# Performance work log

Measured on AMD Instinct MI355X. Metric: run time of the kernel, lower is better.

Reference implementation:

```python
import jax, jax.numpy as jnp
import numpy as np

N = 100000   # nodes
E = 1600000  # edges
F_IN = 128
HID = 128
C = 40
EPS = 1e-5


def setup_inputs() -> dict:
    key = jax.random.key(0)
    ks = jax.random.split(key, 8)
    x = jax.random.normal(ks[0], (N, F_IN), dtype=jnp.float32)
    edge_index = jax.random.randint(ks[1], (2, E), 0, N, dtype=jnp.int32)
    s = 0.05
    return {
        "x": x,
        "edge_index": edge_index,
        "W1": jax.random.normal(ks[2], (F_IN, HID), dtype=jnp.float32) * s,
        "b1": jnp.zeros((HID,), jnp.float32),
        "g1": jnp.ones((HID,), jnp.float32),
        "be1": jnp.zeros((HID,), jnp.float32),
        "W2": jax.random.normal(ks[3], (HID, HID), dtype=jnp.float32) * s,
        "b2": jnp.zeros((HID,), jnp.float32),
        "g2": jnp.ones((HID,), jnp.float32),
        "be2": jnp.zeros((HID,), jnp.float32),
        "W3": jax.random.normal(ks[4], (HID, C), dtype=jnp.float32) * s,
        "b3": jnp.zeros((C,), jnp.float32),
    }


def _gcn_conv(x, W, b, src, dst, deg_inv_sqrt):
    # h = X W; then symmetric-normalized aggregation over edges (incl. self loops)
    h = x @ W                                  # [N, out]
    coef = deg_inv_sqrt[src] * deg_inv_sqrt[dst]  # [E+N]
    msg = h[src] * coef[:, None]               # gather + scale
    out = jax.ops.segment_sum(msg, dst, num_segments=N)
    return out + b


def _batchnorm(x, g, be):
    mean = jnp.mean(x, axis=0)
    var = jnp.mean(jnp.square(x - mean), axis=0)  # biased var (torch BN train)
    return (x - mean) * jax.lax.rsqrt(var + EPS) * g + be


def reference(x, edge_index, W1, b1, g1, be1, W2, b2, g2, be2, W3, b3):
    # add self loops once
    loop = jnp.arange(N, dtype=edge_index.dtype)
    src = jnp.concatenate([edge_index[0], loop])
    dst = jnp.concatenate([edge_index[1], loop])
    deg = jax.ops.segment_sum(jnp.ones_like(dst, dtype=x.dtype), dst, num_segments=N)
    dinv = jax.lax.rsqrt(deg)  # deg >= 1 due to self loops

    h = _gcn_conv(x, W1, b1, src, dst, dinv)
    h = _batchnorm(h, g1, be1)
    h = h + x                      # residual: hidden_dim == num_features
    h = jax.nn.relu(h)             # dropout: eval-mode identity

    h = _gcn_conv(h, W2, b2, src, dst, dinv)
    h = _batchnorm(h, g2, be2)
    h = jax.nn.relu(h)

    h = _gcn_conv(h, W3, b3, src, dst, dinv)
    return jax.nn.log_softmax(h, axis=1)
```

## Files before the change

### kernel.cpp

```cpp
#include <hip/hip_runtime.h>
#include <hip/hip_bf16.h>

#define NN 100000
#define EE 1600000
#define HID 128
#define CLS 40
#define EPSBN 1e-5f
#define NBUK ((NN + 255) >> 8)
#define CAP 6144
#define EPB 4096
#define NPB 512

typedef float f32x4 __attribute__((ext_vector_type(4)));
typedef float f32x2 __attribute__((ext_vector_type(2)));
typedef short s16x8 __attribute__((ext_vector_type(8)));
union U48 { uint4 u; s16x8 s; };

static __device__ __forceinline__ unsigned short f2bf(float f) {
    unsigned u = __float_as_uint(f);
    unsigned r = (u + 0x7fff + ((u >> 16) & 1)) >> 16;
    return (unsigned short)r;
}
static __device__ __forceinline__ unsigned pack2(float a, float b) {
    return (unsigned)f2bf(a) | ((unsigned)f2bf(b) << 16);
}
static __device__ __forceinline__ float bflo(unsigned v) { return __uint_as_float(v << 16); }
static __device__ __forceinline__ float bfhi(unsigned v) { return __uint_as_float(v & 0xffff0000u); }


__global__ void prep_all(const float* __restrict__ W1, const float* __restrict__ W2,
                         const float* __restrict__ W3,
                         unsigned* __restrict__ Wf1, unsigned* __restrict__ Wf2,
                         unsigned* __restrict__ Wf3,
                         int* gcur, float* stats1, float* stats2) {
    int blk = blockIdx.x;
    int tid = threadIdx.x;
    if (blk < 64) {
        const float* W = (blk < 32) ? W1 : W2;
        unsigned* Wf = (blk < 32) ? Wf1 : Wf2;
        int t = ((blk & 31) << 8) + tid;
        int q = t & 3, lane = (t >> 2) & 63, f = t >> 8;
        int ks = f >> 3, ct = f & 7;
        int k = ks * 32 + ((lane >> 4) << 3) + q * 2;
        int col = ct * 16 + (lane & 15);
        Wf[t] = pack2(W[k * 128 + col], W[(k + 1) * 128 + col]);
    } else if (blk < 76) {
        int t = ((blk - 64) << 8) + tid;
        int q = t & 3, lane = (t >> 2) & 63, f = t >> 8;
        int ks = f / 3, ct = f - ks * 3;
        int k = ks * 32 + ((lane >> 4) << 3) + q * 2;
        int col = ct * 16 + (lane & 15);
        float v0 = (col < CLS) ? W3[k * CLS + col] : 0.0f;
        float v1 = (col < CLS) ? W3[(k + 1) * CLS + col] : 0.0f;
        Wf3[t] = pack2(v0, v1);
    } else {
        int j = ((blk - 76) << 8) + tid;
        if (j < NBUK) gcur[j] = j * CAP;
        if (blk == 76) {
            stats1[tid] = 0.0f;
            stats2[tid] = 0.0f;
        }
    }
}


__global__ __launch_bounds__(256) void fill_p1_binned(const int* __restrict__ src,
                                                      const int* __restrict__ dst,
                                                      int* gcur, int* __restrict__ tmp) {
    __shared__ int cnt[NBUK];
    __shared__ int base[NBUK];
    int tid = threadIdx.x;
    for (int j = tid; j < NBUK; j += 256) cnt[j] = 0;
    __syncthreads();

    int es[16], ed[16];
    int i0 = blockIdx.x * EPB;
#pragma unroll
    for (int k = 0; k < 16; k++) {
        int i = i0 + k * 256 + tid;
        bool ok = i < EE;
        es[k] = ok ? src[i] : -1;
        ed[k] = ok ? dst[i] : 0;
        if (ok) atomicAdd(&cnt[ed[k] >> 8], 1);
    }
    __syncthreads();
    for (int j = tid; j < NBUK; j += 256) {
        int c = cnt[j];
        base[j] = c ? atomicAdd(&gcur[j], c) : 0;
        cnt[j] = 0;
    }
    __syncthreads();
#pragma unroll
    for (int k = 0; k < 16; k++) {
        if (es[k] >= 0) {
            int b = ed[k] >> 8;
            int r = atomicAdd(&cnt[b], 1);
            tmp[base[b] + r] = (es[k] << 8) | (ed[k] & 255);
        }
    }
}

__global__ __launch_bounds__(512) void bucket_scan(const int* __restrict__ gcur,
                                                   int* __restrict__ gbase,
                                                   int* __restrict__ row_ptr) {
    __shared__ int sc[512];
    int tid = threadIdx.x;
    int v = (tid < NBUK) ? gcur[tid] - tid * CAP : 0;
    sc[tid] = v;
    __syncthreads();
    for (int off = 1; off < 512; off <<= 1) {
        int t = (tid >= off) ? sc[tid - off] : 0;
        __syncthreads();
        sc[tid] += t;
        __syncthreads();
    }
    if (tid < NBUK) gbase[tid] = sc[tid] - v;
    if (tid == NBUK - 1) {
        gbase[NBUK] = sc[tid];
        row_ptr[NN] = sc[tid];
    }
}

__global__ __launch_bounds__(256) void fill_p2(const int* __restrict__ tmp,
                                               const int* __restrict__ gcur,
                                               const int* __restrict__ gbase,
                                               float* __restrict__ dinv,
                                               int* __restrict__ row_ptr,
                                               int* __restrict__ csr) {
    __shared__ int cnt[256];
    __shared__ int sc[256];
    __shared__ int cur[256];
    int b = blockIdx.x;
    int tid = threadIdx.x;
    int total = gcur[b] - b * CAP;
    cnt[tid] = 0;
    __syncthreads();
    int lo = b * CAP;
    for (int k = tid; k < total; k += 256) atomicAdd(&cnt[tmp[lo + k] & 255], 1);
    __syncthreads();
    int c = cnt[tid];
    sc[tid] = c;
    __syncthreads();
    for (int off = 1; off < 256; off <<= 1) {
        int t = (tid >= off) ? sc[tid - off] : 0;
        __syncthreads();
        sc[tid] += t;
        __syncthreads();
    }
    int node = (b << 8) + tid;
    int rp = gbase[b] + sc[tid] - c;
    if (node < NN) {
        dinv[node] = rsqrtf((float)(c + 1));
        row_ptr[node] = rp;
    }
    cur[tid] = rp;
    __syncthreads();
    for (int k = tid; k < total; k += 256) {
        int v = tmp[lo + k];
        int p = atomicAdd(&cur[v & 255], 1);
        csr[p] = ((unsigned)v) >> 8;
    }
}


template <int MODE>
__global__ __launch_bounds__(256) void gemm128_mfma(const float* __restrict__ Xf,
                                                    const unsigned* __restrict__ Xb,
                                                    const unsigned* __restrict__ Wf,
                                                    const float* __restrict__ stats,
                                                    const float* __restrict__ gam,
                                                    const float* __restrict__ bet,
                                                    const float* __restrict__ xres,
                                                    const float* __restrict__ dinv,
                                                    unsigned char* __restrict__ Hb) {
    int t = threadIdx.x;
    int lane = t & 63, w = t >> 6;
    int wr = w >> 1, wc = w & 1;
    int row_base = blockIdx.x * 64 + wr * 32;

    s16x8 b[4][4];
    const uint4* Wv = (const uint4*)Wf;
#pragma unroll
    for (int ks = 0; ks < 4; ks++)
#pragma unroll
        for (int ct = 0; ct < 4; ct++) {
            int f = ks * 8 + wc * 4 + ct;
            U48 u; u.u = Wv[f * 64 + lane];
            b[ks][ct] = u.s;
        }

    f32x4 acc[2][4] = {};
    int lrow = lane & 15;
    int koff = (lane >> 4) << 3;
    const float invN = 1.0f / (float)NN;

#pragma unroll
    for (int ks = 0; ks < 4; ks++) {
        int k0 = ks * 32 + koff;
        float sc[8], sh[8];
        if (MODE == 1) {
            float4 s0 = *(const float4*)&stats[k0];
            float4 s1 = *(const float4*)&stats[k0 + 4];
            float4 q0 = *(const float4*)&stats[128 + k0];
            float4 q1 = *(const float4*)&stats[128 + k0 + 4];
            float4 g0 = *(const float4*)&gam[k0];
            float4 g1 = *(const float4*)&gam[k0 + 4];
            float4 e0 = *(const float4*)&bet[k0];
            float4 e1 = *(const float4*)&bet[k0 + 4];
            float sv[8] = {s0.x,s0.y,s0.z,s0.w,s1.x,s1.y,s1.z,s1.w};
            float qv[8] = {q0.x,q0.y,q0.z,q0.w,q1.x,q1.y,q1.z,q1.w};
            float gv[8] = {g0.x,g0.y,g0.z,g0.w,g1.x,g1.y,g1.z,g1.w};
            float ev[8] = {e0.x,e0.y,e0.z,e0.w,e1.x,e1.y,e1.z,e1.w};
#pragma unroll
            for (int j = 0; j < 8; j++) {
                float mean = sv[j] * invN;
                float var = qv[j] * invN - mean * mean;
                sc[j] = gv[j] * rsqrtf(var + EPSBN);
                sh[j] = ev[j] - mean * sc[j];
            }
        }
#pragma unroll
        for (int rf = 0; rf < 2; rf++) {
            int row = row_base + rf * 16 + lrow;
            float v[8];
            if (row < NN) {
                if (MODE == 0) {
                    float4 a0 = *(const float4*)&Xf[(size_t)row * 128 + k0];
                    float4 a1 = *(const float4*)&Xf[(size_t)row * 128 + k0 + 4];
                    v[0]=a0.x; v[1]=a0.y; v[2]=a0.z; v[3]=a0.w;
                    v[4]=a1.x; v[5]=a1.y; v[6]=a1.z; v[7]=a1.w;
                } else {
                    uint4 u = *(const uint4*)&Xb[(size_t)row * 64 + k0 / 2];
                    v[0]=bflo(u.x); v[1]=bfhi(u.x); v[2]=bflo(u.y); v[3]=bfhi(u.y);
                    v[4]=bflo(u.z); v[5]=bfhi(u.z); v[6]=bflo(u.w); v[7]=bfhi(u.w);
                    float4 r0 = *(const float4*)&xres[(size_t)row * 128 + k0];
                    float4 r1 = *(const float4*)&xres[(size_t)row * 128 + k0 + 4];
                    float rr[8] = {r0.x,r0.y,r0.z,r0.w,r1.x,r1.y,r1.z,r1.w};
#pragma unroll
                    for (int j = 0; j < 8; j++)
                        v[j] = fmaxf(fmaf(v[j], sc[j], sh[j]) + rr[j], 0.0f);
                }
            } else {
#pragma unroll
                for (int j = 0; j < 8; j++) v[j] = 0.0f;
            }
            U48 a;
            a.u = make_uint4(pack2(v[0], v[1]), pack2(v[2], v[3]),
                             pack2(v[4], v[5]), pack2(v[6], v[7]));
#pragma unroll
            for (int ct = 0; ct < 4; ct++)
                acc[rf][ct] = __builtin_amdgcn_mfma_f32_16x16x32_bf16(a.s, b[ks][ct], acc[rf][ct], 0, 0, 0);
        }
    }

#pragma unroll
    for (int rf = 0; rf < 2; rf++) {
        int rbase = row_base + rf * 16 + ((lane >> 4) << 2);
        float dv[4];
#pragma unroll
        for (int r = 0; r < 4; r++) dv[r] = (rbase + r < NN) ? dinv[rbase + r] : 0.0f;
#pragma unroll
        for (int ct = 0; ct < 4; ct++) {
            int col = wc * 64 + ct * 16 + lrow;
#pragma unroll
            for (int r = 0; r < 4; r++) {
                int row = rbase + r;
                if (row < NN) {
                    int pv = __builtin_amdgcn_cvt_pk_fp8_f32(acc[rf][ct][r] * dv[r], 0.0f, 0, false);
                    Hb[(size_t)row * 128 + col] = (unsigned char)pv;
                }
            }
        }
    }
}

__global__ __launch_bounds__(256) void gemm40_mfma(const unsigned* __restrict__ Xb,
                                                   const unsigned* __restrict__ Wf,
                                                   const float* __restrict__ stats,
                                                   const float* __restrict__ gam,
                                                   const float* __restrict__ bet,
                                                   const float* __restrict__ dinv,
                                                   unsigned char* __restrict__ H3) {
    int t = threadIdx.x;
    int lane = t & 63, w = t >> 6;
    int row_base = blockIdx.x * 64 + w * 16;

    s16x8 b[4][3];
    const uint4* Wv = (const uint4*)Wf;
#pragma unroll
    for (int ks = 0; ks < 4; ks++)
#pragma unroll
        for (int ct = 0; ct < 3; ct++) {
            U48 u; u.u = Wv[(ks * 3 + ct) * 64 + lane];
            b[ks][ct] = u.s;
        }

    f32x4 acc[3] = {};
    int lrow = lane & 15;
    int koff = (lane >> 4) << 3;
    const float invN = 1.0f / (float)NN;

#pragma unroll
    for (int ks = 0; ks < 4; ks++) {
        int k0 = ks * 32 + koff;
        float4 s0 = *(const float4*)&stats[k0];
        float4 s1 = *(const float4*)&stats[k0 + 4];
        float4 q0 = *(const float4*)&stats[128 + k0];
        float4 q1 = *(const float4*)&stats[128 + k0 + 4];
        float4 g0 = *(const float4*)&gam[k0];
        float4 g1 = *(const float4*)&gam[k0 + 4];
        float4 e0 = *(const float4*)&bet[k0];
        float4 e1 = *(const float4*)&bet[k0 + 4];
        float sv[8] = {s0.x,s0.y,s0.z,s0.w,s1.x,s1.y,s1.z,s1.w};
        float qv[8] = {q0.x,q0.y,q0.z,q0.w,q1.x,q1.y,q1.z,q1.w};
        float gv[8] = {g0.x,g0.y,g0.z,g0.w,g1.x,g1.y,g1.z,g1.w};
        float ev[8] = {e0.x,e0.y,e0.z,e0.w,e1.x,e1.y,e1.z,e1.w};
        float sc[8], sh[8];
#pragma unroll
        for (int j = 0; j < 8; j++) {
            float mean = sv[j] * invN;
            float var = qv[j] * invN - mean * mean;
            sc[j] = gv[j] * rsqrtf(var + EPSBN);
            sh[j] = ev[j] - mean * sc[j];
        }
        int row = row_base + lrow;
        float v[8];
        if (row < NN) {
            uint4 u = *(const uint4*)&Xb[(size_t)row * 64 + k0 / 2];
            float av[8] = {bflo(u.x), bfhi(u.x), bflo(u.y), bfhi(u.y),
                           bflo(u.z), bfhi(u.z), bflo(u.w), bfhi(u.w)};
#pragma unroll
            for (int j = 0; j < 8; j++)
                v[j] = fmaxf(fmaf(av[j], sc[j], sh[j]), 0.0f);
        } else {
#pragma unroll
            for (int j = 0; j < 8; j++) v[j] = 0.0f;
        }
        U48 a;
        a.u = make_uint4(pack2(v[0], v[1]), pack2(v[2], v[3]),
                         pack2(v[4], v[5]), pack2(v[6], v[7]));
#pragma unroll
        for (int ct = 0; ct < 3; ct++)
            acc[ct] = __builtin_amdgcn_mfma_f32_16x16x32_bf16(a.s, b[ks][ct], acc[ct], 0, 0, 0);
    }

    int rbase = row_base + ((lane >> 4) << 2);
    float dv[4];
#pragma unroll
    for (int r = 0; r < 4; r++) dv[r] = (rbase + r < NN) ? dinv[rbase + r] : 0.0f;
#pragma unroll
    for (int ct = 0; ct < 3; ct++) {
        int col = ct * 16 + lrow;
        if (col >= CLS) continue;
#pragma unroll
        for (int r = 0; r < 4; r++) {
            int row = rbase + r;
            if (row < NN) {
                int pv = __builtin_amdgcn_cvt_pk_fp8_f32(acc[ct][r] * dv[r], 0.0f, 0, false);
                H3[(size_t)row * CLS + col] = (unsigned char)pv;
            }
        }
    }
}


__global__ __launch_bounds__(256) void agg128_half(const unsigned* __restrict__ h8,
                                                   const int* __restrict__ row_ptr,
                                                   const int* __restrict__ csr,
                                                   const float* __restrict__ dinv,
                                                   const float* __restrict__ bias,
                                                   uint2* __restrict__ outb) {
    int wid = threadIdx.x >> 6;
    int lane = threadIdx.x & 63;
    int half = lane >> 5, l = lane & 31;
    int node = blockIdx.x * 8 + wid * 2 + half;

    unsigned sv = h8[(size_t)node * 32 + l];
    f32x2 alo = __builtin_amdgcn_cvt_pk_f32_fp8(sv, false);
    f32x2 ahi = __builtin_amdgcn_cvt_pk_f32_fp8(sv, true);

    int beg = row_ptr[node], end = row_ptr[node + 1];
    int cnt = end - beg;
    int cmax = max(cnt, __shfl_xor(cnt, 32));

    for (int k = 0; k < cmax; k += 12) {
        int si[12];
        unsigned g[12];
#pragma unroll
        for (int j = 0; j < 12; j++) {
            int idx = beg + k + j;
            si[j] = csr[(idx < end) ? idx : beg];
        }
#pragma unroll
        for (int j = 0; j < 12; j++) {
            int idx = beg + k + j;
            g[j] = (idx < end) ? h8[(size_t)si[j] * 32 + l] : 0u;
        }
#pragma unroll
        for (int j = 0; j < 12; j++) {
            alo += __builtin_amdgcn_cvt_pk_f32_fp8(g[j], false);
            ahi += __builtin_amdgcn_cvt_pk_f32_fp8(g[j], true);
        }
    }

    float di = dinv[node];
    float4 b = *(const float4*)&bias[l * 4];
    outb[(size_t)node * 32 + l] =
        make_uint2(pack2(fmaf(alo.x, di, b.x), fmaf(alo.y, di, b.y)),
                   pack2(fmaf(ahi.x, di, b.z), fmaf(ahi.y, di, b.w)));
}

__global__ __launch_bounds__(256) void agg40_lsm(const unsigned* __restrict__ h3,
                                                 const int* __restrict__ row_ptr,
                                                 const int* __restrict__ csr,
                                                 const float* __restrict__ dinv,
                                                 const float* __restrict__ b3,
                                                 float* __restrict__ out) {
    int wid = threadIdx.x >> 6;
    int lane = threadIdx.x & 63;
    int half = lane >> 5, l30 = lane & 31;
    int slot = l30 / 10;
    int fp = l30 - slot * 10;
    bool sok = slot < 3;
    int node = blockIdx.x * 8 + wid * 2 + half;

    f32x2 alo = {0.0f, 0.0f}, ahi = {0.0f, 0.0f};
    if (slot == 0) {
        unsigned v = h3[(size_t)node * 10 + fp];
        alo = __builtin_amdgcn_cvt_pk_f32_fp8(v, false);
        ahi = __builtin_amdgcn_cvt_pk_f32_fp8(v, true);
    }
    int beg = row_ptr[node], end = row_ptr[node + 1];
    int cnt = end - beg;
    for (int k = 0; k < cnt; k += 12) {
#pragma unroll
        for (int jj = 0; jj < 4; jj++) {
            int idx = beg + k + jj * 3 + slot;
            bool on = sok && (idx < end);
            int s = csr[on ? idx : beg];
            unsigned g = on ? h3[(size_t)s * 10 + fp] : 0u;
            alo += __builtin_amdgcn_cvt_pk_f32_fp8(g, false);
            ahi += __builtin_amdgcn_cvt_pk_f32_fp8(g, true);
        }
    }
    float a0 = alo.x, a1 = alo.y, a2 = ahi.x, a3 = ahi.y;
    float t0 = __shfl(a0, lane + 10), t1 = __shfl(a1, lane + 10);
    float t2 = __shfl(a2, lane + 10), t3 = __shfl(a3, lane + 10);
    float u0 = __shfl(a0, lane + 20), u1 = __shfl(a1, lane + 20);
    float u2 = __shfl(a2, lane + 20), u3 = __shfl(a3, lane + 20);
    bool fin = l30 < 10;
    float l0 = 0.0f, l1 = 0.0f, l2 = 0.0f, l3 = 0.0f;
    if (fin) {
        float di = dinv[node];
        float4 b = *(const float4*)&b3[fp * 4];
        l0 = fmaf(a0 + t0 + u0, di, b.x);
        l1 = fmaf(a1 + t1 + u1, di, b.y);
        l2 = fmaf(a2 + t2 + u2, di, b.z);
        l3 = fmaf(a3 + t3 + u3, di, b.w);
    }
    float m = fin ? fmaxf(fmaxf(l0, l1), fmaxf(l2, l3)) : -1e30f;
#pragma unroll
    for (int off = 16; off > 0; off >>= 1) m = fmaxf(m, __shfl_xor(m, off));
    float s = fin ? (expf(l0 - m) + expf(l1 - m) + expf(l2 - m) + expf(l3 - m)) : 0.0f;
#pragma unroll
    for (int off = 16; off > 0; off >>= 1) s += __shfl_xor(s, off);
    float lse = m + logf(s);
    if (fin)
        *(float4*)&out[(size_t)node * CLS + fp * 4] =
            make_float4(l0 - lse, l1 - lse, l2 - lse, l3 - lse);
}


__global__ __launch_bounds__(256) void bn_part(const uint2* __restrict__ a,
                                               float* __restrict__ gpart, int n) {
    __shared__ float red[4][256];
    int tid = threadIdx.x;
    int w = tid >> 6, lane = tid & 63;
    int half = lane >> 5, l = lane & 31;
    int gw = blockIdx.x * 4 + w;
    float s0 = 0.f, s1 = 0.f, s2 = 0.f, s3 = 0.f;
    float q0 = 0.f, q1 = 0.f, q2 = 0.f, q3 = 0.f;
    int npair = n >> 1;
    for (int p = gw; p < npair; p += NPB * 4) {
        int row = p * 2 + half;
        uint2 u = a[(size_t)row * 32 + l];
        float v0 = bflo(u.x), v1 = bfhi(u.x), v2 = bflo(u.y), v3 = bfhi(u.y);
        s0 += v0; q0 = fmaf(v0, v0, q0);
        s1 += v1; q1 = fmaf(v1, v1, q1);
        s2 += v2; q2 = fmaf(v2, v2, q2);
        s3 += v3; q3 = fmaf(v3, v3, q3);
    }
    s0 += __shfl_xor(s0, 32); s1 += __shfl_xor(s1, 32);
    s2 += __shfl_xor(s2, 32); s3 += __shfl_xor(s3, 32);
    q0 += __shfl_xor(q0, 32); q1 += __shfl_xor(q1, 32);
    q2 += __shfl_xor(q2, 32); q3 += __shfl_xor(q3, 32);
    if (half == 0) {
        red[w][l * 4 + 0] = s0; red[w][l * 4 + 1] = s1;
        red[w][l * 4 + 2] = s2; red[w][l * 4 + 3] = s3;
        red[w][128 + l * 4 + 0] = q0; red[w][128 + l * 4 + 1] = q1;
        red[w][128 + l * 4 + 2] = q2; red[w][128 + l * 4 + 3] = q3;
    }
    __syncthreads();
    float pv = red[0][tid] + red[1][tid] + red[2][tid] + red[3][tid];
    gpart[(size_t)blockIdx.x * 256 + tid] = pv;
}

__global__ __launch_bounds__(256) void bn_final(const float* __restrict__ gpart,
                                                float* __restrict__ stats) {
    int t = threadIdx.x;
    int k0 = blockIdx.x * (NPB / 8);
    float s = 0.0f;
#pragma unroll 8
    for (int k = k0; k < k0 + NPB / 8; k++)
        s += gpart[(size_t)k * 256 + t];
    atomicAdd(&stats[t], s);
}


extern "C" void kernel_launch(void* const* d_in, const int* in_sizes, int n_in,
                              void* d_out, int out_size, void* d_ws, size_t ws_size,
                              hipStream_t stream) {
    const float* x   = (const float*)d_in[0];
    const int*   ei  = (const int*)d_in[1];
    const float* W1  = (const float*)d_in[2];
    const float* b1  = (const float*)d_in[3];
    const float* g1  = (const float*)d_in[4];
    const float* be1 = (const float*)d_in[5];
    const float* W2  = (const float*)d_in[6];
    const float* b2  = (const float*)d_in[7];
    const float* g2  = (const float*)d_in[8];
    const float* be2 = (const float*)d_in[9];
    const float* W3  = (const float*)d_in[10];
    const float* b3  = (const float*)d_in[11];
    float* out = (float*)d_out;

    const int* src = ei;
    const int* dst = ei + EE;

    char* w = (char*)d_ws;
    size_t off = 0;
    auto alloc = [&](size_t bytes) {
        void* p = w + off;
        off += (bytes + 255) & ~(size_t)255;
        return p;
    };
    float* dinv      = (float*)alloc((size_t)NN * 4);
    int*   row_ptr   = (int*)alloc((size_t)(NN + 1) * 4);
    int*   gcur      = (int*)alloc((size_t)NBUK * 4);
    int*   gbase     = (int*)alloc((size_t)(NBUK + 1) * 4);
    int*   tmp       = (int*)alloc((size_t)NBUK * CAP * 4);
    int*   csr       = (int*)alloc((size_t)EE * 4);
    float* stats1    = (float*)alloc(256 * 4);
    float* stats2    = (float*)alloc(256 * 4);
    float* gpart     = (float*)alloc((size_t)NPB * 256 * 4);
    unsigned* Wf1    = (unsigned*)alloc(8192 * 4);
    unsigned* Wf2    = (unsigned*)alloc(8192 * 4);
    unsigned* Wf3    = (unsigned*)alloc(3072 * 4);
    unsigned* aH     = (unsigned*)alloc((size_t)NN * 64 * 4);
    unsigned char* hB8 = (unsigned char*)alloc((size_t)NN * 128);
    unsigned char* h3b = (unsigned char*)alloc((size_t)NN * 40);

    const int NB_P1 = (EE + EPB - 1) / EPB;
    const int NB_G  = (NN + 63) / 64;

    prep_all<<<78, 256, 0, stream>>>(W1, W2, W3, Wf1, Wf2, Wf3, gcur, stats1, stats2);
    fill_p1_binned<<<NB_P1, 256, 0, stream>>>(src, dst, gcur, tmp);
    bucket_scan<<<1, 512, 0, stream>>>(gcur, gbase, row_ptr);
    fill_p2<<<NBUK, 256, 0, stream>>>(tmp, gcur, gbase, dinv, row_ptr, csr);

    gemm128_mfma<0><<<NB_G, 256, 0, stream>>>(x, nullptr, Wf1, nullptr, nullptr, nullptr, nullptr, dinv, hB8);
    agg128_half<<<NN / 8, 256, 0, stream>>>((const unsigned*)hB8, row_ptr, csr, dinv, b1, (uint2*)aH);
    bn_part<<<NPB, 256, 0, stream>>>((const uint2*)aH, gpart, NN);
    bn_final<<<8, 256, 0, stream>>>(gpart, stats1);

    gemm128_mfma<1><<<NB_G, 256, 0, stream>>>(nullptr, aH, Wf2, stats1, g1, be1, x, dinv, hB8);
    agg128_half<<<NN / 8, 256, 0, stream>>>((const unsigned*)hB8, row_ptr, csr, dinv, b2, (uint2*)aH);
    bn_part<<<NPB, 256, 0, stream>>>((const uint2*)aH, gpart, NN);
    bn_final<<<8, 256, 0, stream>>>(gpart, stats2);

    gemm40_mfma<<<NB_G, 256, 0, stream>>>(aH, Wf3, stats2, g2, be2, dinv, h3b);
    agg40_lsm<<<NN / 8, 256, 0, stream>>>((const unsigned*)h3b, row_ptr, csr, dinv, b3, out);
}
```

Measured before the change: 290.1 us.

## Stage GEMM A tiles in LDS with cooperative coalesced loads and shared BN params

Both dense GEMM kernels now load the 64-row input tile cooperatively into padded shared memory with coalesced row-contiguous accesses. The BN-affine, residual and ReLU transform is applied once per element there, and MFMA operands are read from LDS. BN scale and shift are computed once per block into shared arrays instead of per lane per k-step. In gemm128 this also stops the two column-half waves from each reloading and recomputing the same rows. The cost is extra LDS (about 17 KB per block) and two barriers, which may lower occupancy.

```diff
diff --git a/kernel.cpp b/kernel.cpp
--- a/kernel.cpp
+++ b/kernel.cpp
@@ -163,6 +163,8 @@
 }
 
 
+#define LDA 136
+
 template <int MODE>
 __global__ __launch_bounds__(256) void gemm128_mfma(const float* __restrict__ Xf,
                                                     const unsigned* __restrict__ Xb,
@@ -173,10 +175,14 @@
                                                     const float* __restrict__ xres,
                                                     const float* __restrict__ dinv,
                                                     unsigned char* __restrict__ Hb) {
+    __shared__ unsigned short As[64 * LDA];
+    __shared__ float scs[128];
+    __shared__ float shs[128];
     int t = threadIdx.x;
     int lane = t & 63, w = t >> 6;
     int wr = w >> 1, wc = w & 1;
-    int row_base = blockIdx.x * 64 + wr * 32;
+    int blk_row = blockIdx.x * 64;
+    const float invN = 1.0f / (float)NN;
 
     s16x8 b[4][4];
     const uint4* Wv = (const uint4*)Wf;
@@ -189,64 +195,61 @@
             b[ks][ct] = u.s;
         }
 
+    if (MODE == 1) {
+        if (t < 128) {
+            float mean = stats[t] * invN;
+            float var = stats[128 + t] * invN - mean * mean;
+            float sc = gam[t] * rsqrtf(var + EPSBN);
+            scs[t] = sc;
+            shs[t] = bet[t] - mean * sc;
+        }
+        __syncthreads();
+        const uint2* H2 = (const uint2*)Xb;
+        const float4* R4 = (const float4*)xres;
+#pragma unroll
+        for (int i = 0; i < 8; i++) {
+            int idx = i * 256 + t;
+            int row = idx >> 5, c4 = idx & 31;
+            int grow = blk_row + row;
+            uint2 h = make_uint2(0u, 0u);
+            float4 r = make_float4(0, 0, 0, 0);
+            if (grow < NN) {
+                h = H2[(size_t)grow * 32 + c4];
+                r = R4[(size_t)grow * 32 + c4];
+            }
+            int f0 = c4 * 4;
+            float v0 = fmaxf(fmaf(bflo(h.x), scs[f0 + 0], shs[f0 + 0]) + r.x, 0.0f);
+            float v1 = fmaxf(fmaf(bfhi(h.x), scs[f0 + 1], shs[f0 + 1]) + r.y, 0.0f);
+            float v2 = fmaxf(fmaf(bflo(h.y), scs[f0 + 2], shs[f0 + 2]) + r.z, 0.0f);
+            float v3 = fmaxf(fmaf(bfhi(h.y), scs[f0 + 3], shs[f0 + 3]) + r.w, 0.0f);
+            *(uint2*)&As[row * LDA + c4 * 4] = make_uint2(pack2(v0, v1), pack2(v2, v3));
+        }
+    } else {
+        const float4* X4 = (const float4*)Xf;
+#pragma unroll
+        for (int i = 0; i < 8; i++) {
+            int idx = i * 256 + t;
+            int row = idx >> 5, c4 = idx & 31;
+            int grow = blk_row + row;
+            float4 a = make_float4(0, 0, 0, 0);
+            if (grow < NN) a = X4[(size_t)grow * 32 + c4];
+            *(uint2*)&As[row * LDA + c4 * 4] = make_uint2(pack2(a.x, a.y), pack2(a.z, a.w));
+        }
+    }
+    __syncthreads();
+
     f32x4 acc[2][4] = {};
     int lrow = lane & 15;
     int koff = (lane >> 4) << 3;
-    const float invN = 1.0f / (float)NN;
 
 #pragma unroll
     for (int ks = 0; ks < 4; ks++) {
         int k0 = ks * 32 + koff;
-        float sc[8], sh[8];
-        if (MODE == 1) {
-            float4 s0 = *(const float4*)&stats[k0];
-            float4 s1 = *(const float4*)&stats[k0 + 4];
-            float4 q0 = *(const float4*)&stats[128 + k0];
-            float4 q1 = *(const float4*)&stats[128 + k0 + 4];
-            float4 g0 = *(const float4*)&gam[k0];
-            float4 g1 = *(const float4*)&gam[k0 + 4];
-            float4 e0 = *(const float4*)&bet[k0];
-            float4 e1 = *(const float4*)&bet[k0 + 4];
-            float sv[8] = {s0.x,s0.y,s0.z,s0.w,s1.x,s1.y,s1.z,s1.w};
-            float qv[8] = {q0.x,q0.y,q0.z,q0.w,q1.x,q1.y,q1.z,q1.w};
-            float gv[8] = {g0.x,g0.y,g0.z,g0.w,g1.x,g1.y,g1.z,g1.w};
-            float ev[8] = {e0.x,e0.y,e0.z,e0.w,e1.x,e1.y,e1.z,e1.w};
-#pragma unroll
-            for (int j = 0; j < 8; j++) {
-                float mean = sv[j] * invN;
-                float var = qv[j] * invN - mean * mean;
-                sc[j] = gv[j] * rsqrtf(var + EPSBN);
-                sh[j] = ev[j] - mean * sc[j];
-            }
-        }
 #pragma unroll
         for (int rf = 0; rf < 2; rf++) {
-            int row = row_base + rf * 16 + lrow;
-            float v[8];
-            if (row < NN) {
-                if (MODE == 0) {
-                    float4 a0 = *(const float4*)&Xf[(size_t)row * 128 + k0];
-                    float4 a1 = *(const float4*)&Xf[(size_t)row * 128 + k0 + 4];
-                    v[0]=a0.x; v[1]=a0.y; v[2]=a0.z; v[3]=a0.w;
-                    v[4]=a1.x; v[5]=a1.y; v[6]=a1.z; v[7]=a1.w;
-                } else {
-                    uint4 u = *(const uint4*)&Xb[(size_t)row * 64 + k0 / 2];
-                    v[0]=bflo(u.x); v[1]=bfhi(u.x); v[2]=bflo(u.y); v[3]=bfhi(u.y);
-                    v[4]=bflo(u.z); v[5]=bfhi(u.z); v[6]=bflo(u.w); v[7]=bfhi(u.w);
-                    float4 r0 = *(const float4*)&xres[(size_t)row * 128 + k0];
-                    float4 r1 = *(const float4*)&xres[(size_t)row * 128 + k0 + 4];
-                    float rr[8] = {r0.x,r0.y,r0.z,r0.w,r1.x,r1.y,r1.z,r1.w};
-#pragma unroll
-                    for (int j = 0; j < 8; j++)
-                        v[j] = fmaxf(fmaf(v[j], sc[j], sh[j]) + rr[j], 0.0f);
-                }
-            } else {
-#pragma unroll
-                for (int j = 0; j < 8; j++) v[j] = 0.0f;
-            }
+            int rloc = wr * 32 + rf * 16 + lrow;
             U48 a;
-            a.u = make_uint4(pack2(v[0], v[1]), pack2(v[2], v[3]),
-                             pack2(v[4], v[5]), pack2(v[6], v[7]));
+            a.u = *(const uint4*)&As[rloc * LDA + k0];
 #pragma unroll
             for (int ct = 0; ct < 4; ct++)
                 acc[rf][ct] = __builtin_amdgcn_mfma_f32_16x16x32_bf16(a.s, b[ks][ct], acc[rf][ct], 0, 0, 0);
@@ -255,7 +258,7 @@
 
 #pragma unroll
     for (int rf = 0; rf < 2; rf++) {
-        int rbase = row_base + rf * 16 + ((lane >> 4) << 2);
+        int rbase = blk_row + wr * 32 + rf * 16 + ((lane >> 4) << 2);
         float dv[4];
 #pragma unroll
         for (int r = 0; r < 4; r++) dv[r] = (rbase + r < NN) ? dinv[rbase + r] : 0.0f;
@@ -281,9 +284,13 @@
                                                    const float* __restrict__ bet,
                                                    const float* __restrict__ dinv,
                                                    unsigned char* __restrict__ H3) {
+    __shared__ unsigned short As[64 * LDA];
+    __shared__ float scs[128];
+    __shared__ float shs[128];
     int t = threadIdx.x;
     int lane = t & 63, w = t >> 6;
-    int row_base = blockIdx.x * 64 + w * 16;
+    int blk_row = blockIdx.x * 64;
+    const float invN = 1.0f / (float)NN;
 
     s16x8 b[4][3];
     const uint4* Wv = (const uint4*)Wf;
@@ -295,56 +302,47 @@
             b[ks][ct] = u.s;
         }
 
+    if (t < 128) {
+        float mean = stats[t] * invN;
+        float var = stats[128 + t] * invN - mean * mean;
+        float sc = gam[t] * rsqrtf(var + EPSBN);
+        scs[t] = sc;
+        shs[t] = bet[t] - mean * sc;
+    }
+    __syncthreads();
+    const uint2* H2 = (const uint2*)Xb;
+#pragma unroll
+    for (int i = 0; i < 8; i++) {
+        int idx = i * 256 + t;
+        int row = idx >> 5, c4 = idx & 31;
+        int grow = blk_row + row;
+        uint2 h = make_uint2(0u, 0u);
+        if (grow < NN) h = H2[(size_t)grow * 32 + c4];
+        int f0 = c4 * 4;
+        float v0 = fmaxf(fmaf(bflo(h.x), scs[f0 + 0], shs[f0 + 0]), 0.0f);
+        float v1 = fmaxf(fmaf(bfhi(h.x), scs[f0 + 1], shs[f0 + 1]), 0.0f);
+        float v2 = fmaxf(fmaf(bflo(h.y), scs[f0 + 2], shs[f0 + 2]), 0.0f);
+        float v3 = fmaxf(fmaf(bfhi(h.y), scs[f0 + 3], shs[f0 + 3]), 0.0f);
+        *(uint2*)&As[row * LDA + c4 * 4] = make_uint2(pack2(v0, v1), pack2(v2, v3));
+    }
+    __syncthreads();
+
     f32x4 acc[3] = {};
     int lrow = lane & 15;
     int koff = (lane >> 4) << 3;
-    const float invN = 1.0f / (float)NN;
 
 #pragma unroll
     for (int ks = 0; ks < 4; ks++) {
         int k0 = ks * 32 + koff;
-        float4 s0 = *(const float4*)&stats[k0];
-        float4 s1 = *(const float4*)&stats[k0 + 4];
-        float4 q0 = *(const float4*)&stats[128 + k0];
-        float4 q1 = *(const float4*)&stats[128 + k0 + 4];
-        float4 g0 = *(const float4*)&gam[k0];
-        float4 g1 = *(const float4*)&gam[k0 + 4];
-        float4 e0 = *(const float4*)&bet[k0];
-        float4 e1 = *(const float4*)&bet[k0 + 4];
-        float sv[8] = {s0.x,s0.y,s0.z,s0.w,s1.x,s1.y,s1.z,s1.w};
-        float qv[8] = {q0.x,q0.y,q0.z,q0.w,q1.x,q1.y,q1.z,q1.w};
-        float gv[8] = {g0.x,g0.y,g0.z,g0.w,g1.x,g1.y,g1.z,g1.w};
-        float ev[8] = {e0.x,e0.y,e0.z,e0.w,e1.x,e1.y,e1.z,e1.w};
-        float sc[8], sh[8];
-#pragma unroll
-        for (int j = 0; j < 8; j++) {
-            float mean = sv[j] * invN;
-            float var = qv[j] * invN - mean * mean;
-            sc[j] = gv[j] * rsqrtf(var + EPSBN);
-            sh[j] = ev[j] - mean * sc[j];
-        }
-        int row = row_base + lrow;
-        float v[8];
-        if (row < NN) {
-            uint4 u = *(const uint4*)&Xb[(size_t)row * 64 + k0 / 2];
-            float av[8] = {bflo(u.x), bfhi(u.x), bflo(u.y), bfhi(u.y),
-                           bflo(u.z), bfhi(u.z), bflo(u.w), bfhi(u.w)};
-#pragma unroll
-            for (int j = 0; j < 8; j++)
-                v[j] = fmaxf(fmaf(av[j], sc[j], sh[j]), 0.0f);
-        } else {
-#pragma unroll
-            for (int j = 0; j < 8; j++) v[j] = 0.0f;
-        }
+        int rloc = w * 16 + lrow;
         U48 a;
-        a.u = make_uint4(pack2(v[0], v[1]), pack2(v[2], v[3]),
-                         pack2(v[4], v[5]), pack2(v[6], v[7]));
+        a.u = *(const uint4*)&As[rloc * LDA + k0];
 #pragma unroll
         for (int ct = 0; ct < 3; ct++)
             acc[ct] = __builtin_amdgcn_mfma_f32_16x16x32_bf16(a.s, b[ks][ct], acc[ct], 0, 0, 0);
     }
 
-    int rbase = row_base + ((lane >> 4) << 2);
+    int rbase = blk_row + w * 16 + ((lane >> 4) << 2);
     float dv[4];
 #pragma unroll
     for (int r = 0; r < 4; r++) dv[r] = (rbase + r < NN) ? dinv[rbase + r] : 0.0f;
```

After: 267.8 us. 1.08x faster.
